# Kernel tuning notes

Hardware: AMD Instinct MI355X
Metric: run time of the kernel (lower is better)

The kernel has to match this reference:

```python
import jax, jax.numpy as jnp
import numpy as np

BOOST_STRENGTH = 1.0  # from init kwargs, already >= 0


def setup_inputs() -> dict:
    key = jax.random.key(0)
    k1, k2 = jax.random.split(key)
    B, C, H, W = 64, 128, 56, 56
    x = jax.random.normal(k1, (B, C, H, W), dtype=jnp.float32)
    # duty cycles are running activation frequencies in [0, 1]
    duty_cycles = jax.random.uniform(k2, (1, C, 1, 1), dtype=jnp.float32)
    k = 40141  # round(0.1 * C*H*W)
    return {"x": x, "duty_cycles": duty_cycles, "k": k}


def reference(x, duty_cycles, k):
    B = x.shape[0]
    n = x.shape[1] * x.shape[2] * x.shape[3]
    target_density = jnp.float32(k / n)
    # boosting only selects winners; original (unboosted) values are kept
    boost_factors = jnp.exp((target_density - duty_cycles) * BOOST_STRENGTH)
    boosted = (x * boost_factors).reshape(B, -1)   # [B, n]
    flat_x = x.reshape(B, -1)                      # [B, n]
    _, idx = jax.lax.top_k(boosted, k)             # [B, k]
    winners = jnp.take_along_axis(flat_x, idx, axis=1)  # original values at winning units
    res = jnp.zeros_like(flat_x).at[jnp.arange(B)[:, None], idx].set(winners)
    return res.reshape(x.shape)
```

## Files before the change

kernel.cpp:

```cpp
#include <hip/hip_runtime.h>
#include <stdint.h>

#define BB 64
#define CC 128
#define HW 3136
#define NPR (CC * HW)
#define NBINS 8192
#define BIN_SHIFT 19
#define KEY_LOW 0x7FFFFu

typedef float vf4 __attribute__((ext_vector_type(4)));

#define ROWMETA_OFF 512
#define COUNTER_OFF 2048
#define HIST_OFF 4096
#define CAND_OFF (HIST_OFF + (size_t)BB * NBINS * 4)

__device__ __forceinline__ uint32_t tokey(float b) {
    uint32_t u = __float_as_uint(b);
    return u ^ (uint32_t)(((int32_t)u >> 31) | 0x80000000);
}

__device__ __forceinline__ float boostf(const float* dc, int c, int K) {
    float td = (float)((double)K / (double)NPR);
    float d = td - dc[c];
    return (float)exp((double)d);
}

__global__ __launch_bounds__(256) void k_hist(const float* __restrict__ x,
                                              const float* __restrict__ dc,
                                              const int* __restrict__ kptr,
                                              uint32_t* __restrict__ hist) {
    __shared__ uint32_t lh[NBINS];
    __shared__ float sbf[8];
    for (int i = threadIdx.x; i < NBINS; i += 256) lh[i] = 0;
    if (threadIdx.x < 8) {
        int c0 = (blockIdx.x & 15) * 8;
        sbf[threadIdx.x] = boostf(dc, c0 + threadIdx.x, *kptr);
    }
    __syncthreads();

    int row = blockIdx.x >> 4;
    int c0 = (blockIdx.x & 15) * 8;
    const float4* xp = (const float4*)(x + (size_t)row * NPR + (size_t)c0 * HW);
    const int nf4 = 8 * HW / 4;

    int t = threadIdx.x;
    for (; t + 256 < nf4; t += 512) {
        float4 a = xp[t];
        float4 b = xp[t + 256];
        float fa = sbf[t / 784];
        float fb = sbf[(t + 256) / 784];
        atomicAdd(&lh[tokey(a.x * fa) >> BIN_SHIFT], 1u);
        atomicAdd(&lh[tokey(a.y * fa) >> BIN_SHIFT], 1u);
        atomicAdd(&lh[tokey(a.z * fa) >> BIN_SHIFT], 1u);
        atomicAdd(&lh[tokey(a.w * fa) >> BIN_SHIFT], 1u);
        atomicAdd(&lh[tokey(b.x * fb) >> BIN_SHIFT], 1u);
        atomicAdd(&lh[tokey(b.y * fb) >> BIN_SHIFT], 1u);
        atomicAdd(&lh[tokey(b.z * fb) >> BIN_SHIFT], 1u);
        atomicAdd(&lh[tokey(b.w * fb) >> BIN_SHIFT], 1u);
    }
    if (t < nf4) {
        float4 a = xp[t];
        float fa = sbf[t / 784];
        atomicAdd(&lh[tokey(a.x * fa) >> BIN_SHIFT], 1u);
        atomicAdd(&lh[tokey(a.y * fa) >> BIN_SHIFT], 1u);
        atomicAdd(&lh[tokey(a.z * fa) >> BIN_SHIFT], 1u);
        atomicAdd(&lh[tokey(a.w * fa) >> BIN_SHIFT], 1u);
    }
    __syncthreads();
    uint32_t* gh = hist + (size_t)row * NBINS;
    for (int i = threadIdx.x; i < NBINS; i += 256) {
        uint32_t v = lh[i];
        if (v) atomicAdd(&gh[i], v);
    }
}

__global__ __launch_bounds__(256) void k_scan(const uint32_t* __restrict__ hist,
                                              const int* __restrict__ kptr,
                                              int2* __restrict__ rowmeta) {
    int row = blockIdx.x;
    const uint32_t* gh = hist + (size_t)row * NBINS;
    uint32_t K = (uint32_t)(*kptr);
    __shared__ uint32_t csum[256];
    int t = threadIdx.x;
    int hi = NBINS - 1 - 32 * t;
    uint32_t s = 0;
    for (int j = 0; j < 32; j++) s += gh[hi - j];
    csum[t] = s;
    __syncthreads();
    for (int off = 1; off < 256; off <<= 1) {
        uint32_t v = (t >= off) ? csum[t - off] : 0u;
        __syncthreads();
        csum[t] += v;
        __syncthreads();
    }
    uint32_t incl = csum[t];
    uint32_t excl = incl - s;
    if (excl < K && incl >= K) {
        uint32_t cum = excl;
        for (int j = 0; j < 32; j++) {
            int b = hi - j;
            uint32_t h = gh[b];
            if (cum + h >= K) { rowmeta[row] = make_int2(b, (int)(K - cum)); break; }
            cum += h;
        }
    }
}

__global__ __launch_bounds__(256) void k_write(const float* __restrict__ x,
                                               const float* __restrict__ dc,
                                               const int* __restrict__ kptr,
                                               const int2* __restrict__ rowmeta,
                                               float* __restrict__ out,
                                               unsigned long long* __restrict__ cand,
                                               uint32_t* __restrict__ counters,
                                               int cap) {
    int row = blockIdx.x >> 4;
    int c0 = (blockIdx.x & 15) * 8;
    int bstar = rowmeta[row].x;

    __shared__ float sbf[8];
    __shared__ uint32_t lcnt;
    __shared__ uint32_t gbase;
    __shared__ unsigned long long lbuf[2048];
    if (threadIdx.x == 0) lcnt = 0;
    if (threadIdx.x < 8) sbf[threadIdx.x] = boostf(dc, c0 + threadIdx.x, *kptr);
    __syncthreads();

    size_t base = (size_t)row * NPR + (size_t)c0 * HW;
    const float4* xp = (const float4*)(x + base);
    vf4* op = (vf4*)(out + base);
    int jbase = c0 * HW;
    const int nf4 = 8 * HW / 4;

    int t = threadIdx.x;
    for (; t + 256 < nf4; t += 512) {
        float4 a = xp[t];
        float4 b = xp[t + 256];
        float fa = sbf[t / 784];
        float fb = sbf[(t + 256) / 784];
        vf4 oa, ob;
        float* ai = (float*)&a;
        float* bi = (float*)&b;
        #pragma unroll
        for (int q = 0; q < 4; q++) {
            float xv = ai[q];
            uint32_t key = tokey(xv * fa);
            int bin = (int)(key >> BIN_SHIFT);
            oa[q] = (bin > bstar) ? xv : 0.0f;
            if (bin == bstar) {
                uint32_t j = (uint32_t)(jbase + 4 * t + q);
                unsigned long long packed =
                    ((unsigned long long)(key & KEY_LOW) << 32) | (uint32_t)(~j);
                uint32_t pos = atomicAdd(&lcnt, 1u);
                if (pos < 2048u) lbuf[pos] = packed;
                else {
                    uint32_t gp = atomicAdd(&counters[row], 1u);
                    if ((int)gp < cap) cand[(size_t)row * cap + gp] = packed;
                }
            }
        }
        #pragma unroll
        for (int q = 0; q < 4; q++) {
            float xv = bi[q];
            uint32_t key = tokey(xv * fb);
            int bin = (int)(key >> BIN_SHIFT);
            ob[q] = (bin > bstar) ? xv : 0.0f;
            if (bin == bstar) {
                uint32_t j = (uint32_t)(jbase + 4 * (t + 256) + q);
                unsigned long long packed =
                    ((unsigned long long)(key & KEY_LOW) << 32) | (uint32_t)(~j);
                uint32_t pos = atomicAdd(&lcnt, 1u);
                if (pos < 2048u) lbuf[pos] = packed;
                else {
                    uint32_t gp = atomicAdd(&counters[row], 1u);
                    if ((int)gp < cap) cand[(size_t)row * cap + gp] = packed;
                }
            }
        }
        __builtin_nontemporal_store(oa, &op[t]);
        __builtin_nontemporal_store(ob, &op[t + 256]);
    }
    if (t < nf4) {
        float4 a = xp[t];
        float fa = sbf[t / 784];
        vf4 oa;
        float* ai = (float*)&a;
        #pragma unroll
        for (int q = 0; q < 4; q++) {
            float xv = ai[q];
            uint32_t key = tokey(xv * fa);
            int bin = (int)(key >> BIN_SHIFT);
            oa[q] = (bin > bstar) ? xv : 0.0f;
            if (bin == bstar) {
                uint32_t j = (uint32_t)(jbase + 4 * t + q);
                unsigned long long packed =
                    ((unsigned long long)(key & KEY_LOW) << 32) | (uint32_t)(~j);
                uint32_t pos = atomicAdd(&lcnt, 1u);
                if (pos < 2048u) lbuf[pos] = packed;
                else {
                    uint32_t gp = atomicAdd(&counters[row], 1u);
                    if ((int)gp < cap) cand[(size_t)row * cap + gp] = packed;
                }
            }
        }
        __builtin_nontemporal_store(oa, &op[t]);
    }
    __syncthreads();
    uint32_t m = lcnt < 2048u ? lcnt : 2048u;
    if (threadIdx.x == 0) gbase = atomicAdd(&counters[row], m);
    __syncthreads();
    for (uint32_t i = threadIdx.x; i < m; i += 256) {
        uint32_t pos = gbase + i;
        if ((int)pos < cap) cand[(size_t)row * cap + pos] = lbuf[i];
    }
}

__global__ __launch_bounds__(1024) void k_select(const float* __restrict__ x,
                                                 float* __restrict__ out,
                                                 const unsigned long long* __restrict__ cand,
                                                 const uint32_t* __restrict__ counters,
                                                 const int2* __restrict__ rowmeta,
                                                 int cap) {
    int row = blockIdx.x;
    uint32_t cnt = counters[row];
    if ((int)cnt > cap) cnt = (uint32_t)cap;
    int E = rowmeta[row].y;
    const unsigned long long* cp = cand + (size_t)row * cap;
    int tid = threadIdx.x;

    __shared__ uint32_t hist[256];
    __shared__ uint32_t sufs[256];
    __shared__ unsigned long long buf[6144];
    __shared__ uint32_t scnt;
    __shared__ int sh_d, sh_done;

    unsigned long long prefix = 0ull, mask = 0ull, thr = 0ull;
    uint32_t remaining = (uint32_t)E;
    bool compacted = false;
    uint32_t csize = cnt;
    if (tid == 0) sh_done = 0;

    for (int shift = 48; shift >= 0; shift -= 8) {
        if (tid < 256) hist[tid] = 0;
        __syncthreads();
        if (!compacted) {
            for (uint32_t s = tid; s < cnt; s += 1024) {
                unsigned long long v = cp[s];
                if ((v & mask) == prefix)
                    atomicAdd(&hist[(uint32_t)(v >> shift) & 255u], 1u);
            }
        } else {
            for (uint32_t s = tid; s < csize; s += 1024)
                atomicAdd(&hist[(uint32_t)(buf[s] >> shift) & 255u], 1u);
        }
        __syncthreads();
        if (tid < 256) sufs[tid] = hist[tid];
        __syncthreads();
        for (int off = 1; off < 256; off <<= 1) {
            uint32_t add = 0;
            if (tid < 256 && tid + off < 256) add = sufs[tid + off];
            __syncthreads();
            if (tid < 256) sufs[tid] += add;
            __syncthreads();
        }
        if (tid < 256) {
            uint32_t sd = sufs[tid];
            uint32_t sn = (tid < 255) ? sufs[tid + 1] : 0u;
            if (sd >= remaining && sn < remaining) sh_d = tid;
        }
        __syncthreads();
        int d = sh_d;
        uint32_t cumG = (d < 255) ? sufs[d + 1] : 0u;
        uint32_t binC = sufs[d] - cumG;
        unsigned long long npref = prefix | ((unsigned long long)(uint32_t)d << shift);
        bool done = (sufs[d] == remaining);
        if (done) {
            thr = npref;
            if (tid == 0) sh_done = 1;
        }
        remaining -= cumG;
        __syncthreads();
        if (!sh_done && binC <= 6144u && shift > 0) {
            if (tid == 0) scnt = 0;
            unsigned long long keep[6]; int nk = 0;
            if (compacted) {
                for (uint32_t s = tid; s < csize; s += 1024) {
                    unsigned long long v = buf[s];
                    if (((uint32_t)(v >> shift) & 255u) == (uint32_t)d) {
                        if (nk < 6) keep[nk++] = v;
                    }
                }
            }
            __syncthreads();
            if (!compacted) {
                for (uint32_t s = tid; s < cnt; s += 1024) {
                    unsigned long long v = cp[s];
                    if ((v & mask) == prefix &&
                        ((uint32_t)(v >> shift) & 255u) == (uint32_t)d) {
                        uint32_t p = atomicAdd(&scnt, 1u);
                        buf[p] = v;
                    }
                }
            } else if (nk > 0) {
                uint32_t p = atomicAdd(&scnt, (uint32_t)nk);
                for (int i = 0; i < nk; i++) buf[p + i] = keep[i];
            }
            __syncthreads();
            csize = binC;
            compacted = true;
        }
        prefix = npref;
        mask |= (0xFFull << shift);
        if (sh_done) break;
    }
    if (!sh_done) thr = prefix;

    const float* xr = x + (size_t)row * NPR;
    float* orow = out + (size_t)row * NPR;
    for (uint32_t s = tid; s < cnt; s += 1024) {
        unsigned long long v = cp[s];
        if (v >= thr) {
            uint32_t j = ~(uint32_t)v;
            orow[j] = xr[j];
        }
    }
}

extern "C" void kernel_launch(void* const* d_in, const int* in_sizes, int n_in,
                              void* d_out, int out_size, void* d_ws, size_t ws_size,
                              hipStream_t stream) {
    const float* x  = (const float*)d_in[0];
    const float* dc = (const float*)d_in[1];
    const int* kptr = (const int*)d_in[2];
    float* out = (float*)d_out;

    char* ws = (char*)d_ws;
    int2* rowmeta       = (int2*)(ws + ROWMETA_OFF);
    uint32_t* counters  = (uint32_t*)(ws + COUNTER_OFF);
    uint32_t* hist      = (uint32_t*)(ws + HIST_OFF);
    unsigned long long* cand = (unsigned long long*)(ws + CAND_OFF);

    size_t cap_sz = (ws_size > CAND_OFF) ? (ws_size - CAND_OFF) / ((size_t)BB * 8) : 0;
    if (cap_sz > 65536) cap_sz = 65536;
    int cap = (int)cap_sz;

    (void)hipMemsetAsync(ws, 0, CAND_OFF, stream);
    k_hist<<<BB * 16, 256, 0, stream>>>(x, dc, kptr, hist);
    k_scan<<<BB, 256, 0, stream>>>(hist, kptr, rowmeta);
    k_write<<<BB * 16, 256, 0, stream>>>(x, dc, kptr, rowmeta, out, cand, counters, cap);
    k_select<<<BB, 1024, 0, stream>>>(x, out, cand, counters, rowmeta, cap);
}
```

Baseline: 243.2 us.

## Fuse histogram, scan, write and select into one cooperative kernel

Replaces the memset plus four separate kernel launches with a single cooperative kernel that uses grid-wide syncs between phases: zeroing, histogram, per-row threshold scan, masked write, and radix select. It removes the launch gaps and the separate memset, and reuses one shared-memory union across phases. The select phase now runs with 256 threads and a smaller compaction buffer instead of 1024 threads, and grid.sync costs plus an occupancy limit of 1024 co-resident blocks are added. If the cooperative launch fails, the code falls back to the old path.

Result: slower. 611.2 us (+151.3%).

```diff
diff --git a/kernel.cpp b/kernel.cpp
--- a/kernel.cpp
+++ b/kernel.cpp
@@ -1,5 +1,8 @@
 #include <hip/hip_runtime.h>
+#include <hip/hip_cooperative_groups.h>
 #include <stdint.h>
+
+namespace cg = cooperative_groups;
 
 #define BB 64
 #define CC 128
@@ -8,6 +11,8 @@
 #define NBINS 8192
 #define BIN_SHIFT 19
 #define KEY_LOW 0x7FFFFu
+#define GRID (BB * 16)
+#define SELCAP 4096
 
 typedef float vf4 __attribute__((ext_vector_type(4)));
 
@@ -25,6 +30,285 @@
     float td = (float)((double)K / (double)NPR);
     float d = td - dc[c];
     return (float)exp((double)d);
+}
+
+union SMem {
+    struct { uint32_t lh[NBINS]; float sbf[8]; } h;
+    struct { uint32_t csum[256]; } sc;
+    struct { float sbf[8]; uint32_t lcnt, gbase;
+             unsigned long long lbuf[2048]; } w;
+    struct { uint32_t hist[256]; uint32_t sufs[256];
+             unsigned long long buf[SELCAP];
+             uint32_t scnt; int sh_d, sh_done; } s;
+};
+
+__global__ __launch_bounds__(256, 4) void k_fused(const float* __restrict__ x,
+                                                  const float* __restrict__ dc,
+                                                  const int* __restrict__ kptr,
+                                                  float* __restrict__ out,
+                                                  unsigned long long* __restrict__ cand,
+                                                  uint32_t* __restrict__ counters,
+                                                  uint32_t* __restrict__ hist,
+                                                  int2* __restrict__ rowmeta,
+                                                  int cap) {
+    cg::grid_group grid = cg::this_grid();
+    __shared__ SMem sm;
+    const int tid = threadIdx.x;
+    const int blk = blockIdx.x;
+    const int row = blk >> 4;
+    const int c0 = (blk & 15) * 8;
+    const int K = *kptr;
+    const int nf4 = 8 * HW / 4;
+
+    {
+        const int total = BB * NBINS;
+        for (int i = blk * 256 + tid; i < total; i += GRID * 256) hist[i] = 0;
+        if (blk == 0 && tid < BB) { counters[tid] = 0u; rowmeta[tid] = make_int2(0, 0); }
+    }
+    grid.sync();
+
+    {
+        for (int i = tid; i < NBINS; i += 256) sm.h.lh[i] = 0;
+        if (tid < 8) sm.h.sbf[tid] = boostf(dc, c0 + tid, K);
+        __syncthreads();
+        const float4* xp = (const float4*)(x + (size_t)row * NPR + (size_t)c0 * HW);
+        int t = tid;
+        for (; t + 256 < nf4; t += 512) {
+            float4 a = xp[t];
+            float4 b = xp[t + 256];
+            float fa = sm.h.sbf[t / 784];
+            float fb = sm.h.sbf[(t + 256) / 784];
+            atomicAdd(&sm.h.lh[tokey(a.x * fa) >> BIN_SHIFT], 1u);
+            atomicAdd(&sm.h.lh[tokey(a.y * fa) >> BIN_SHIFT], 1u);
+            atomicAdd(&sm.h.lh[tokey(a.z * fa) >> BIN_SHIFT], 1u);
+            atomicAdd(&sm.h.lh[tokey(a.w * fa) >> BIN_SHIFT], 1u);
+            atomicAdd(&sm.h.lh[tokey(b.x * fb) >> BIN_SHIFT], 1u);
+            atomicAdd(&sm.h.lh[tokey(b.y * fb) >> BIN_SHIFT], 1u);
+            atomicAdd(&sm.h.lh[tokey(b.z * fb) >> BIN_SHIFT], 1u);
+            atomicAdd(&sm.h.lh[tokey(b.w * fb) >> BIN_SHIFT], 1u);
+        }
+        if (t < nf4) {
+            float4 a = xp[t];
+            float fa = sm.h.sbf[t / 784];
+            atomicAdd(&sm.h.lh[tokey(a.x * fa) >> BIN_SHIFT], 1u);
+            atomicAdd(&sm.h.lh[tokey(a.y * fa) >> BIN_SHIFT], 1u);
+            atomicAdd(&sm.h.lh[tokey(a.z * fa) >> BIN_SHIFT], 1u);
+            atomicAdd(&sm.h.lh[tokey(a.w * fa) >> BIN_SHIFT], 1u);
+        }
+        __syncthreads();
+        uint32_t* gh = hist + (size_t)row * NBINS;
+        for (int i = tid; i < NBINS; i += 256) {
+            uint32_t v = sm.h.lh[i];
+            if (v) atomicAdd(&gh[i], v);
+        }
+    }
+    grid.sync();
+
+    if (blk < BB) {
+        const uint32_t* gh = hist + (size_t)blk * NBINS;
+        uint32_t Ku = (uint32_t)K;
+        int hi = NBINS - 1 - 32 * tid;
+        uint32_t ssum = 0;
+        for (int j = 0; j < 32; j++) ssum += gh[hi - j];
+        sm.sc.csum[tid] = ssum;
+        __syncthreads();
+        for (int off = 1; off < 256; off <<= 1) {
+            uint32_t v = (tid >= off) ? sm.sc.csum[tid - off] : 0u;
+            __syncthreads();
+            sm.sc.csum[tid] += v;
+            __syncthreads();
+        }
+        uint32_t incl = sm.sc.csum[tid];
+        uint32_t excl = incl - ssum;
+        if (excl < Ku && incl >= Ku) {
+            uint32_t cum = excl;
+            for (int j = 0; j < 32; j++) {
+                int b = hi - j;
+                uint32_t h = gh[b];
+                if (cum + h >= Ku) { rowmeta[blk] = make_int2(b, (int)(Ku - cum)); break; }
+                cum += h;
+            }
+        }
+    }
+    grid.sync();
+
+    {
+        int bstar = rowmeta[row].x;
+        if (tid == 0) sm.w.lcnt = 0;
+        if (tid < 8) sm.w.sbf[tid] = boostf(dc, c0 + tid, K);
+        __syncthreads();
+
+        size_t base = (size_t)row * NPR + (size_t)c0 * HW;
+        const float4* xp = (const float4*)(x + base);
+        vf4* op = (vf4*)(out + base);
+        int jbase = c0 * HW;
+
+        int t = tid;
+        for (; t + 256 < nf4; t += 512) {
+            float4 a = xp[t];
+            float4 b = xp[t + 256];
+            float fa = sm.w.sbf[t / 784];
+            float fb = sm.w.sbf[(t + 256) / 784];
+            vf4 oa, ob;
+            float* ai = (float*)&a;
+            float* bi = (float*)&b;
+            #pragma unroll
+            for (int q = 0; q < 4; q++) {
+                float xv = ai[q];
+                uint32_t key = tokey(xv * fa);
+                int bin = (int)(key >> BIN_SHIFT);
+                oa[q] = (bin > bstar) ? xv : 0.0f;
+                if (bin == bstar) {
+                    uint32_t j = (uint32_t)(jbase + 4 * t + q);
+                    unsigned long long packed =
+                        ((unsigned long long)(key & KEY_LOW) << 32) | (uint32_t)(~j);
+                    uint32_t pos = atomicAdd(&sm.w.lcnt, 1u);
+                    if (pos < 2048u) sm.w.lbuf[pos] = packed;
+                    else {
+                        uint32_t gp = atomicAdd(&counters[row], 1u);
+                        if ((int)gp < cap) cand[(size_t)row * cap + gp] = packed;
+                    }
+                }
+            }
+            #pragma unroll
+            for (int q = 0; q < 4; q++) {
+                float xv = bi[q];
+                uint32_t key = tokey(xv * fb);
+                int bin = (int)(key >> BIN_SHIFT);
+                ob[q] = (bin > bstar) ? xv : 0.0f;
+                if (bin == bstar) {
+                    uint32_t j = (uint32_t)(jbase + 4 * (t + 256) + q);
+                    unsigned long long packed =
+                        ((unsigned long long)(key & KEY_LOW) << 32) | (uint32_t)(~j);
+                    uint32_t pos = atomicAdd(&sm.w.lcnt, 1u);
+                    if (pos < 2048u) sm.w.lbuf[pos] = packed;
+                    else {
+                        uint32_t gp = atomicAdd(&counters[row], 1u);
+                        if ((int)gp < cap) cand[(size_t)row * cap + gp] = packed;
+                    }
+                }
+            }
+            __builtin_nontemporal_store(oa, &op[t]);
+            __builtin_nontemporal_store(ob, &op[t + 256]);
+        }
+        if (t < nf4) {
+            float4 a = xp[t];
+            float fa = sm.w.sbf[t / 784];
+            vf4 oa;
+            float* ai = (float*)&a;
+            #pragma unroll
+            for (int q = 0; q < 4; q++) {
+                float xv = ai[q];
+                uint32_t key = tokey(xv * fa);
+                int bin = (int)(key >> BIN_SHIFT);
+                oa[q] = (bin > bstar) ? xv : 0.0f;
+                if (bin == bstar) {
+                    uint32_t j = (uint32_t)(jbase + 4 * t + q);
+                    unsigned long long packed =
+                        ((unsigned long long)(key & KEY_LOW) << 32) | (uint32_t)(~j);
+                    uint32_t pos = atomicAdd(&sm.w.lcnt, 1u);
+                    if (pos < 2048u) sm.w.lbuf[pos] = packed;
+                    else {
+                        uint32_t gp = atomicAdd(&counters[row], 1u);
+                        if ((int)gp < cap) cand[(size_t)row * cap + gp] = packed;
+                    }
+                }
+            }
+            __builtin_nontemporal_store(oa, &op[t]);
+        }
+        __syncthreads();
+        uint32_t m = sm.w.lcnt < 2048u ? sm.w.lcnt : 2048u;
+        if (tid == 0) sm.w.gbase = atomicAdd(&counters[row], m);
+        __syncthreads();
+        for (uint32_t i = tid; i < m; i += 256) {
+            uint32_t pos = sm.w.gbase + i;
+            if ((int)pos < cap) cand[(size_t)row * cap + pos] = sm.w.lbuf[i];
+        }
+    }
+    grid.sync();
+
+    if (blk < BB) {
+        uint32_t cnt = counters[blk];
+        if ((int)cnt > cap) cnt = (uint32_t)cap;
+        int E = rowmeta[blk].y;
+        const unsigned long long* cp = cand + (size_t)blk * cap;
+
+        unsigned long long prefix = 0ull, mask = 0ull, thr = 0ull;
+        uint32_t remaining = (uint32_t)E;
+        bool compacted = false;
+        uint32_t csize = cnt;
+        if (tid == 0) sm.s.sh_done = 0;
+
+        for (int shift = 48; shift >= 0; shift -= 8) {
+            sm.s.hist[tid] = 0;
+            __syncthreads();
+            if (!compacted) {
+                for (uint32_t s = tid; s < cnt; s += 256) {
+                    unsigned long long v = cp[s];
+                    if ((v & mask) == prefix)
+                        atomicAdd(&sm.s.hist[(uint32_t)(v >> shift) & 255u], 1u);
+                }
+            } else {
+                for (uint32_t s = tid; s < csize; s += 256)
+                    atomicAdd(&sm.s.hist[(uint32_t)(sm.s.buf[s] >> shift) & 255u], 1u);
+            }
+            __syncthreads();
+            sm.s.sufs[tid] = sm.s.hist[tid];
+            __syncthreads();
+            for (int off = 1; off < 256; off <<= 1) {
+                uint32_t add = (tid + off < 256) ? sm.s.sufs[tid + off] : 0u;
+                __syncthreads();
+                sm.s.sufs[tid] += add;
+                __syncthreads();
+            }
+            {
+                uint32_t sd = sm.s.sufs[tid];
+                uint32_t sn = (tid < 255) ? sm.s.sufs[tid + 1] : 0u;
+                if (sd >= remaining && sn < remaining) sm.s.sh_d = tid;
+            }
+            __syncthreads();
+            int d = sm.s.sh_d;
+            uint32_t cumG = (d < 255) ? sm.s.sufs[d + 1] : 0u;
+            uint32_t binC = sm.s.sufs[d] - cumG;
+            unsigned long long npref = prefix | ((unsigned long long)(uint32_t)d << shift);
+            unsigned long long nmask = mask | (0xFFull << shift);
+            bool done = (sm.s.sufs[d] == remaining);
+            if (done) {
+                thr = npref;
+                if (tid == 0) sm.s.sh_done = 1;
+            }
+            remaining -= cumG;
+            __syncthreads();
+            if (!sm.s.sh_done && binC <= (uint32_t)SELCAP && shift > 0) {
+                if (tid == 0) sm.s.scnt = 0;
+                __syncthreads();
+                for (uint32_t s = tid; s < cnt; s += 256) {
+                    unsigned long long v = cp[s];
+                    if ((v & nmask) == npref) {
+                        uint32_t p = atomicAdd(&sm.s.scnt, 1u);
+                        sm.s.buf[p] = v;
+                    }
+                }
+                __syncthreads();
+                csize = binC;
+                compacted = true;
+            }
+            prefix = npref;
+            mask = nmask;
+            if (sm.s.sh_done) break;
+        }
+        if (!sm.s.sh_done) thr = prefix;
+
+        const float* xr = x + (size_t)blk * NPR;
+        float* orow = out + (size_t)blk * NPR;
+        for (uint32_t s = tid; s < cnt; s += 256) {
+            unsigned long long v = cp[s];
+            if (v >= thr) {
+                uint32_t j = ~(uint32_t)v;
+                orow[j] = xr[j];
+            }
+        }
+    }
 }
 
 __global__ __launch_bounds__(256) void k_hist(const float* __restrict__ x,
@@ -39,12 +323,10 @@
         sbf[threadIdx.x] = boostf(dc, c0 + threadIdx.x, *kptr);
     }
     __syncthreads();
-
     int row = blockIdx.x >> 4;
     int c0 = (blockIdx.x & 15) * 8;
     const float4* xp = (const float4*)(x + (size_t)row * NPR + (size_t)c0 * HW);
     const int nf4 = 8 * HW / 4;
-
     int t = threadIdx.x;
     for (; t + 256 < nf4; t += 512) {
         float4 a = xp[t];
@@ -119,7 +401,6 @@
     int row = blockIdx.x >> 4;
     int c0 = (blockIdx.x & 15) * 8;
     int bstar = rowmeta[row].x;
-
     __shared__ float sbf[8];
     __shared__ uint32_t lcnt;
     __shared__ uint32_t gbase;
@@ -127,13 +408,11 @@
     if (threadIdx.x == 0) lcnt = 0;
     if (threadIdx.x < 8) sbf[threadIdx.x] = boostf(dc, c0 + threadIdx.x, *kptr);
     __syncthreads();
-
     size_t base = (size_t)row * NPR + (size_t)c0 * HW;
     const float4* xp = (const float4*)(x + base);
     vf4* op = (vf4*)(out + base);
     int jbase = c0 * HW;
     const int nf4 = 8 * HW / 4;
-
     int t = threadIdx.x;
     for (; t + 256 < nf4; t += 512) {
         float4 a = xp[t];
@@ -229,19 +508,16 @@
     int E = rowmeta[row].y;
     const unsigned long long* cp = cand + (size_t)row * cap;
     int tid = threadIdx.x;
-
     __shared__ uint32_t hist[256];
     __shared__ uint32_t sufs[256];
     __shared__ unsigned long long buf[6144];
     __shared__ uint32_t scnt;
     __shared__ int sh_d, sh_done;
-
     unsigned long long prefix = 0ull, mask = 0ull, thr = 0ull;
     uint32_t remaining = (uint32_t)E;
     bool compacted = false;
     uint32_t csize = cnt;
     if (tid == 0) sh_done = 0;
-
     for (int shift = 48; shift >= 0; shift -= 8) {
         if (tid < 256) hist[tid] = 0;
         __syncthreads();
@@ -316,7 +592,6 @@
         if (sh_done) break;
     }
     if (!sh_done) thr = prefix;
-
     const float* xr = x + (size_t)row * NPR;
     float* orow = out + (size_t)row * NPR;
     for (uint32_t s = tid; s < cnt; s += 1024) {
@@ -346,9 +621,15 @@
     if (cap_sz > 65536) cap_sz = 65536;
     int cap = (int)cap_sz;
 
-    (void)hipMemsetAsync(ws, 0, CAND_OFF, stream);
-    k_hist<<<BB * 16, 256, 0, stream>>>(x, dc, kptr, hist);
-    k_scan<<<BB, 256, 0, stream>>>(hist, kptr, rowmeta);
-    k_write<<<BB * 16, 256, 0, stream>>>(x, dc, kptr, rowmeta, out, cand, counters, cap);
-    k_select<<<BB, 1024, 0, stream>>>(x, out, cand, counters, rowmeta, cap);
-}
+    void* args[] = {(void*)&x, (void*)&dc, (void*)&kptr, (void*)&out, (void*)&cand,
+                    (void*)&counters, (void*)&hist, (void*)&rowmeta, (void*)&cap};
+    hipError_t err = hipLaunchCooperativeKernel((void*)k_fused, dim3(GRID), dim3(256),
+                                                args, 0, stream);
+    if (err != hipSuccess) {
+        (void)hipMemsetAsync(ws, 0, CAND_OFF, stream);
+        k_hist<<<BB * 16, 256, 0, stream>>>(x, dc, kptr, hist);
+        k_scan<<<BB, 256, 0, stream>>>(hist, kptr, rowmeta);
+        k_write<<<BB * 16, 256, 0, stream>>>(x, dc, kptr, rowmeta, out, cand, counters, cap);
+        k_select<<<BB, 1024, 0, stream>>>(x, out, cand, counters, rowmeta, cap);
+    }
+}
```

## Fuse scan into histogram and selection into write via last-block completion counters

Applied to the files above, without the earlier changes.

Merges the per-row scan into the histogram kernel and the candidate radix-select into the write kernel. Per-row arrival counters with threadfence let the last of each row's 16 blocks do the follow-up step, cutting the launch count from four to two. The local histogram also packs two 16-bit bins per 32-bit word, halving shared memory, and the select stage now runs in 256 threads with a smaller 2048-entry compaction buffer. The trade-off is that the tail work for a row runs in one 256-thread block instead of a 1024-thread block, and more often has to re-read candidates from global memory.

New measurement: 391.7 us. 61.0% more time.

```diff
diff --git a/kernel.cpp b/kernel.cpp
--- a/kernel.cpp
+++ b/kernel.cpp
@@ -8,11 +8,14 @@
 #define NBINS 8192
 #define BIN_SHIFT 19
 #define KEY_LOW 0x7FFFFu
+#define SELCAP 2048
 
 typedef float vf4 __attribute__((ext_vector_type(4)));
 
 #define ROWMETA_OFF 512
+#define HARR_OFF 1536
 #define COUNTER_OFF 2048
+#define WARR_OFF 2560
 #define HIST_OFF 4096
 #define CAND_OFF (HIST_OFF + (size_t)BB * NBINS * 4)
 
@@ -27,105 +30,121 @@
     return (float)exp((double)d);
 }
 
-__global__ __launch_bounds__(256) void k_hist(const float* __restrict__ x,
-                                              const float* __restrict__ dc,
-                                              const int* __restrict__ kptr,
-                                              uint32_t* __restrict__ hist) {
-    __shared__ uint32_t lh[NBINS];
+__device__ __forceinline__ uint32_t aload32(const uint32_t* p) {
+    return __hip_atomic_load(p, __ATOMIC_RELAXED, __HIP_MEMORY_SCOPE_AGENT);
+}
+__device__ __forceinline__ unsigned long long aload64(const unsigned long long* p) {
+    return __hip_atomic_load(p, __ATOMIC_RELAXED, __HIP_MEMORY_SCOPE_AGENT);
+}
+__device__ __forceinline__ void astore64(unsigned long long* p, unsigned long long v) {
+    __hip_atomic_store(p, v, __ATOMIC_RELAXED, __HIP_MEMORY_SCOPE_AGENT);
+}
+
+__global__ __launch_bounds__(256) void k_hist_scan(const float* __restrict__ x,
+                                                   const float* __restrict__ dc,
+                                                   const int* __restrict__ kptr,
+                                                   uint32_t* __restrict__ hist,
+                                                   uint32_t* __restrict__ harr,
+                                                   int2* __restrict__ rowmeta) {
+    __shared__ uint32_t lh32[NBINS / 2];
     __shared__ float sbf[8];
-    for (int i = threadIdx.x; i < NBINS; i += 256) lh[i] = 0;
-    if (threadIdx.x < 8) {
-        int c0 = (blockIdx.x & 15) * 8;
-        sbf[threadIdx.x] = boostf(dc, c0 + threadIdx.x, *kptr);
-    }
-    __syncthreads();
-
-    int row = blockIdx.x >> 4;
-    int c0 = (blockIdx.x & 15) * 8;
+    __shared__ int lastflag;
+    const int tid = threadIdx.x;
+    const int row = blockIdx.x >> 4;
+    const int c0 = (blockIdx.x & 15) * 8;
+    const int K = *kptr;
+
+    for (int i = tid; i < NBINS / 2; i += 256) lh32[i] = 0;
+    if (tid < 8) sbf[tid] = boostf(dc, c0 + tid, K);
+    __syncthreads();
+
     const float4* xp = (const float4*)(x + (size_t)row * NPR + (size_t)c0 * HW);
     const int nf4 = 8 * HW / 4;
-
-    int t = threadIdx.x;
+    int t = tid;
     for (; t + 256 < nf4; t += 512) {
         float4 a = xp[t];
         float4 b = xp[t + 256];
         float fa = sbf[t / 784];
         float fb = sbf[(t + 256) / 784];
-        atomicAdd(&lh[tokey(a.x * fa) >> BIN_SHIFT], 1u);
-        atomicAdd(&lh[tokey(a.y * fa) >> BIN_SHIFT], 1u);
-        atomicAdd(&lh[tokey(a.z * fa) >> BIN_SHIFT], 1u);
-        atomicAdd(&lh[tokey(a.w * fa) >> BIN_SHIFT], 1u);
-        atomicAdd(&lh[tokey(b.x * fb) >> BIN_SHIFT], 1u);
-        atomicAdd(&lh[tokey(b.y * fb) >> BIN_SHIFT], 1u);
-        atomicAdd(&lh[tokey(b.z * fb) >> BIN_SHIFT], 1u);
-        atomicAdd(&lh[tokey(b.w * fb) >> BIN_SHIFT], 1u);
+        uint32_t bx;
+        bx = tokey(a.x * fa) >> BIN_SHIFT; atomicAdd(&lh32[bx >> 1], 1u << ((bx & 1) << 4));
+        bx = tokey(a.y * fa) >> BIN_SHIFT; atomicAdd(&lh32[bx >> 1], 1u << ((bx & 1) << 4));
+        bx = tokey(a.z * fa) >> BIN_SHIFT; atomicAdd(&lh32[bx >> 1], 1u << ((bx & 1) << 4));
+        bx = tokey(a.w * fa) >> BIN_SHIFT; atomicAdd(&lh32[bx >> 1], 1u << ((bx & 1) << 4));
+        bx = tokey(b.x * fb) >> BIN_SHIFT; atomicAdd(&lh32[bx >> 1], 1u << ((bx & 1) << 4));
+        bx = tokey(b.y * fb) >> BIN_SHIFT; atomicAdd(&lh32[bx >> 1], 1u << ((bx & 1) << 4));
+        bx = tokey(b.z * fb) >> BIN_SHIFT; atomicAdd(&lh32[bx >> 1], 1u << ((bx & 1) << 4));
+        bx = tokey(b.w * fb) >> BIN_SHIFT; atomicAdd(&lh32[bx >> 1], 1u << ((bx & 1) << 4));
     }
     if (t < nf4) {
         float4 a = xp[t];
         float fa = sbf[t / 784];
-        atomicAdd(&lh[tokey(a.x * fa) >> BIN_SHIFT], 1u);
-        atomicAdd(&lh[tokey(a.y * fa) >> BIN_SHIFT], 1u);
-        atomicAdd(&lh[tokey(a.z * fa) >> BIN_SHIFT], 1u);
-        atomicAdd(&lh[tokey(a.w * fa) >> BIN_SHIFT], 1u);
+        uint32_t bx;
+        bx = tokey(a.x * fa) >> BIN_SHIFT; atomicAdd(&lh32[bx >> 1], 1u << ((bx & 1) << 4));
+        bx = tokey(a.y * fa) >> BIN_SHIFT; atomicAdd(&lh32[bx >> 1], 1u << ((bx & 1) << 4));
+        bx = tokey(a.z * fa) >> BIN_SHIFT; atomicAdd(&lh32[bx >> 1], 1u << ((bx & 1) << 4));
+        bx = tokey(a.w * fa) >> BIN_SHIFT; atomicAdd(&lh32[bx >> 1], 1u << ((bx & 1) << 4));
     }
     __syncthreads();
     uint32_t* gh = hist + (size_t)row * NBINS;
-    for (int i = threadIdx.x; i < NBINS; i += 256) {
-        uint32_t v = lh[i];
-        if (v) atomicAdd(&gh[i], v);
-    }
-}
-
-__global__ __launch_bounds__(256) void k_scan(const uint32_t* __restrict__ hist,
-                                              const int* __restrict__ kptr,
-                                              int2* __restrict__ rowmeta) {
-    int row = blockIdx.x;
-    const uint32_t* gh = hist + (size_t)row * NBINS;
-    uint32_t K = (uint32_t)(*kptr);
-    __shared__ uint32_t csum[256];
-    int t = threadIdx.x;
-    int hi = NBINS - 1 - 32 * t;
-    uint32_t s = 0;
-    for (int j = 0; j < 32; j++) s += gh[hi - j];
-    csum[t] = s;
+    for (int i = tid; i < NBINS / 2; i += 256) {
+        uint32_t w = lh32[i];
+        if (w & 0xFFFFu) atomicAdd(&gh[2 * i], w & 0xFFFFu);
+        if (w >> 16)     atomicAdd(&gh[2 * i + 1], w >> 16);
+    }
+    __threadfence();
+    if (tid == 0) lastflag = (atomicAdd(&harr[row], 1u) == 15u);
+    __syncthreads();
+    if (!lastflag) return;
+
+    uint32_t* csum = lh32;
+    uint32_t Ku = (uint32_t)K;
+    int hi = NBINS - 1 - 32 * tid;
+    uint32_t ssum = 0;
+    for (int j = 0; j < 32; j++) ssum += aload32(&gh[hi - j]);
+    csum[tid] = ssum;
     __syncthreads();
     for (int off = 1; off < 256; off <<= 1) {
-        uint32_t v = (t >= off) ? csum[t - off] : 0u;
-        __syncthreads();
-        csum[t] += v;
-        __syncthreads();
-    }
-    uint32_t incl = csum[t];
-    uint32_t excl = incl - s;
-    if (excl < K && incl >= K) {
+        uint32_t v = (tid >= off) ? csum[tid - off] : 0u;
+        __syncthreads();
+        csum[tid] += v;
+        __syncthreads();
+    }
+    uint32_t incl = csum[tid];
+    uint32_t excl = incl - ssum;
+    if (excl < Ku && incl >= Ku) {
         uint32_t cum = excl;
         for (int j = 0; j < 32; j++) {
             int b = hi - j;
-            uint32_t h = gh[b];
-            if (cum + h >= K) { rowmeta[row] = make_int2(b, (int)(K - cum)); break; }
+            uint32_t h = aload32(&gh[b]);
+            if (cum + h >= Ku) { rowmeta[row] = make_int2(b, (int)(Ku - cum)); break; }
             cum += h;
         }
     }
 }
 
-__global__ __launch_bounds__(256) void k_write(const float* __restrict__ x,
-                                               const float* __restrict__ dc,
-                                               const int* __restrict__ kptr,
-                                               const int2* __restrict__ rowmeta,
-                                               float* __restrict__ out,
-                                               unsigned long long* __restrict__ cand,
-                                               uint32_t* __restrict__ counters,
-                                               int cap) {
-    int row = blockIdx.x >> 4;
-    int c0 = (blockIdx.x & 15) * 8;
-    int bstar = rowmeta[row].x;
+__global__ __launch_bounds__(256) void k_write_sel(const float* __restrict__ x,
+                                                   const float* __restrict__ dc,
+                                                   const int* __restrict__ kptr,
+                                                   const int2* __restrict__ rowmeta,
+                                                   float* __restrict__ out,
+                                                   unsigned long long* __restrict__ cand,
+                                                   uint32_t* __restrict__ counters,
+                                                   uint32_t* __restrict__ warr,
+                                                   int cap) {
+    const int tid = threadIdx.x;
+    const int row = blockIdx.x >> 4;
+    const int c0 = (blockIdx.x & 15) * 8;
+    const int bstar = rowmeta[row].x;
 
     __shared__ float sbf[8];
-    __shared__ uint32_t lcnt;
-    __shared__ uint32_t gbase;
-    __shared__ unsigned long long lbuf[2048];
-    if (threadIdx.x == 0) lcnt = 0;
-    if (threadIdx.x < 8) sbf[threadIdx.x] = boostf(dc, c0 + threadIdx.x, *kptr);
+    __shared__ uint32_t lcnt, gbase;
+    __shared__ unsigned long long lbuf[SELCAP];
+    __shared__ uint32_t shist[256], ssufs[256];
+    __shared__ uint32_t scnt;
+    __shared__ int sh_d, sh_done, lastflag;
+    if (tid == 0) lcnt = 0;
+    if (tid < 8) sbf[tid] = boostf(dc, c0 + tid, *kptr);
     __syncthreads();
 
     size_t base = (size_t)row * NPR + (size_t)c0 * HW;
@@ -134,7 +153,7 @@
     int jbase = c0 * HW;
     const int nf4 = 8 * HW / 4;
 
-    int t = threadIdx.x;
+    int t = tid;
     for (; t + 256 < nf4; t += 512) {
         float4 a = xp[t];
         float4 b = xp[t + 256];
@@ -154,10 +173,10 @@
                 unsigned long long packed =
                     ((unsigned long long)(key & KEY_LOW) << 32) | (uint32_t)(~j);
                 uint32_t pos = atomicAdd(&lcnt, 1u);
-                if (pos < 2048u) lbuf[pos] = packed;
+                if (pos < (uint32_t)SELCAP) lbuf[pos] = packed;
                 else {
                     uint32_t gp = atomicAdd(&counters[row], 1u);
-                    if ((int)gp < cap) cand[(size_t)row * cap + gp] = packed;
+                    if ((int)gp < cap) astore64(&cand[(size_t)row * cap + gp], packed);
                 }
             }
         }
@@ -172,10 +191,10 @@
                 unsigned long long packed =
                     ((unsigned long long)(key & KEY_LOW) << 32) | (uint32_t)(~j);
                 uint32_t pos = atomicAdd(&lcnt, 1u);
-                if (pos < 2048u) lbuf[pos] = packed;
+                if (pos < (uint32_t)SELCAP) lbuf[pos] = packed;
                 else {
                     uint32_t gp = atomicAdd(&counters[row], 1u);
-                    if ((int)gp < cap) cand[(size_t)row * cap + gp] = packed;
+                    if ((int)gp < cap) astore64(&cand[(size_t)row * cap + gp], packed);
                 }
             }
         }
@@ -198,43 +217,32 @@
                 unsigned long long packed =
                     ((unsigned long long)(key & KEY_LOW) << 32) | (uint32_t)(~j);
                 uint32_t pos = atomicAdd(&lcnt, 1u);
-                if (pos < 2048u) lbuf[pos] = packed;
+                if (pos < (uint32_t)SELCAP) lbuf[pos] = packed;
                 else {
                     uint32_t gp = atomicAdd(&counters[row], 1u);
-                    if ((int)gp < cap) cand[(size_t)row * cap + gp] = packed;
+                    if ((int)gp < cap) astore64(&cand[(size_t)row * cap + gp], packed);
                 }
             }
         }
         __builtin_nontemporal_store(oa, &op[t]);
     }
     __syncthreads();
-    uint32_t m = lcnt < 2048u ? lcnt : 2048u;
-    if (threadIdx.x == 0) gbase = atomicAdd(&counters[row], m);
-    __syncthreads();
-    for (uint32_t i = threadIdx.x; i < m; i += 256) {
+    uint32_t m = lcnt < (uint32_t)SELCAP ? lcnt : (uint32_t)SELCAP;
+    if (tid == 0) gbase = atomicAdd(&counters[row], m);
+    __syncthreads();
+    for (uint32_t i = tid; i < m; i += 256) {
         uint32_t pos = gbase + i;
-        if ((int)pos < cap) cand[(size_t)row * cap + pos] = lbuf[i];
-    }
-}
-
-__global__ __launch_bounds__(1024) void k_select(const float* __restrict__ x,
-                                                 float* __restrict__ out,
-                                                 const unsigned long long* __restrict__ cand,
-                                                 const uint32_t* __restrict__ counters,
-                                                 const int2* __restrict__ rowmeta,
-                                                 int cap) {
-    int row = blockIdx.x;
-    uint32_t cnt = counters[row];
+        if ((int)pos < cap) astore64(&cand[(size_t)row * cap + pos], lbuf[i]);
+    }
+    __threadfence();
+    if (tid == 0) lastflag = (atomicAdd(&warr[row], 1u) == 15u);
+    __syncthreads();
+    if (!lastflag) return;
+
+    uint32_t cnt = aload32(&counters[row]);
     if ((int)cnt > cap) cnt = (uint32_t)cap;
     int E = rowmeta[row].y;
     const unsigned long long* cp = cand + (size_t)row * cap;
-    int tid = threadIdx.x;
-
-    __shared__ uint32_t hist[256];
-    __shared__ uint32_t sufs[256];
-    __shared__ unsigned long long buf[6144];
-    __shared__ uint32_t scnt;
-    __shared__ int sh_d, sh_done;
 
     unsigned long long prefix = 0ull, mask = 0ull, thr = 0ull;
     uint32_t remaining = (uint32_t)E;
@@ -243,84 +251,69 @@
     if (tid == 0) sh_done = 0;
 
     for (int shift = 48; shift >= 0; shift -= 8) {
-        if (tid < 256) hist[tid] = 0;
+        shist[tid] = 0;
         __syncthreads();
         if (!compacted) {
-            for (uint32_t s = tid; s < cnt; s += 1024) {
-                unsigned long long v = cp[s];
+            for (uint32_t s = tid; s < cnt; s += 256) {
+                unsigned long long v = aload64(&cp[s]);
                 if ((v & mask) == prefix)
-                    atomicAdd(&hist[(uint32_t)(v >> shift) & 255u], 1u);
+                    atomicAdd(&shist[(uint32_t)(v >> shift) & 255u], 1u);
             }
         } else {
-            for (uint32_t s = tid; s < csize; s += 1024)
-                atomicAdd(&hist[(uint32_t)(buf[s] >> shift) & 255u], 1u);
-        }
-        __syncthreads();
-        if (tid < 256) sufs[tid] = hist[tid];
+            for (uint32_t s = tid; s < csize; s += 256)
+                atomicAdd(&shist[(uint32_t)(lbuf[s] >> shift) & 255u], 1u);
+        }
+        __syncthreads();
+        ssufs[tid] = shist[tid];
         __syncthreads();
         for (int off = 1; off < 256; off <<= 1) {
-            uint32_t add = 0;
-            if (tid < 256 && tid + off < 256) add = sufs[tid + off];
+            uint32_t add = (tid + off < 256) ? ssufs[tid + off] : 0u;
             __syncthreads();
-            if (tid < 256) sufs[tid] += add;
+            ssufs[tid] += add;
             __syncthreads();
         }
-        if (tid < 256) {
-            uint32_t sd = sufs[tid];
-            uint32_t sn = (tid < 255) ? sufs[tid + 1] : 0u;
+        {
+            uint32_t sd = ssufs[tid];
+            uint32_t sn = (tid < 255) ? ssufs[tid + 1] : 0u;
             if (sd >= remaining && sn < remaining) sh_d = tid;
         }
         __syncthreads();
         int d = sh_d;
-        uint32_t cumG = (d < 255) ? sufs[d + 1] : 0u;
-        uint32_t binC = sufs[d] - cumG;
+        uint32_t cumG = (d < 255) ? ssufs[d + 1] : 0u;
+        uint32_t binC = ssufs[d] - cumG;
         unsigned long long npref = prefix | ((unsigned long long)(uint32_t)d << shift);
-        bool done = (sufs[d] == remaining);
+        unsigned long long nmask = mask | (0xFFull << shift);
+        bool done = (ssufs[d] == remaining);
         if (done) {
             thr = npref;
             if (tid == 0) sh_done = 1;
         }
         remaining -= cumG;
         __syncthreads();
-        if (!sh_done && binC <= 6144u && shift > 0) {
+        if (!sh_done && binC <= (uint32_t)SELCAP && shift > 0) {
             if (tid == 0) scnt = 0;
-            unsigned long long keep[6]; int nk = 0;
-            if (compacted) {
-                for (uint32_t s = tid; s < csize; s += 1024) {
-                    unsigned long long v = buf[s];
-                    if (((uint32_t)(v >> shift) & 255u) == (uint32_t)d) {
-                        if (nk < 6) keep[nk++] = v;
-                    }
+            __syncthreads();
+            for (uint32_t s = tid; s < cnt; s += 256) {
+                unsigned long long v = aload64(&cp[s]);
+                if ((v & nmask) == npref) {
+                    uint32_t p = atomicAdd(&scnt, 1u);
+                    lbuf[p] = v;
                 }
-            }
-            __syncthreads();
-            if (!compacted) {
-                for (uint32_t s = tid; s < cnt; s += 1024) {
-                    unsigned long long v = cp[s];
-                    if ((v & mask) == prefix &&
-                        ((uint32_t)(v >> shift) & 255u) == (uint32_t)d) {
-                        uint32_t p = atomicAdd(&scnt, 1u);
-                        buf[p] = v;
-                    }
-                }
-            } else if (nk > 0) {
-                uint32_t p = atomicAdd(&scnt, (uint32_t)nk);
-                for (int i = 0; i < nk; i++) buf[p + i] = keep[i];
             }
             __syncthreads();
             csize = binC;
             compacted = true;
         }
         prefix = npref;
-        mask |= (0xFFull << shift);
+        mask = nmask;
         if (sh_done) break;
     }
     if (!sh_done) thr = prefix;
 
     const float* xr = x + (size_t)row * NPR;
     float* orow = out + (size_t)row * NPR;
-    for (uint32_t s = tid; s < cnt; s += 1024) {
-        unsigned long long v = cp[s];
+    for (uint32_t s = tid; s < cnt; s += 256) {
+        unsigned long long v = aload64(&cp[s]);
         if (v >= thr) {
             uint32_t j = ~(uint32_t)v;
             orow[j] = xr[j];
@@ -338,7 +331,9 @@
 
     char* ws = (char*)d_ws;
     int2* rowmeta       = (int2*)(ws + ROWMETA_OFF);
+    uint32_t* harr      = (uint32_t*)(ws + HARR_OFF);
     uint32_t* counters  = (uint32_t*)(ws + COUNTER_OFF);
+    uint32_t* warr      = (uint32_t*)(ws + WARR_OFF);
     uint32_t* hist      = (uint32_t*)(ws + HIST_OFF);
     unsigned long long* cand = (unsigned long long*)(ws + CAND_OFF);
 
@@ -347,8 +342,7 @@
     int cap = (int)cap_sz;
 
     (void)hipMemsetAsync(ws, 0, CAND_OFF, stream);
-    k_hist<<<BB * 16, 256, 0, stream>>>(x, dc, kptr, hist);
-    k_scan<<<BB, 256, 0, stream>>>(hist, kptr, rowmeta);
-    k_write<<<BB * 16, 256, 0, stream>>>(x, dc, kptr, rowmeta, out, cand, counters, cap);
-    k_select<<<BB, 1024, 0, stream>>>(x, out, cand, counters, rowmeta, cap);
-}
+    k_hist_scan<<<BB * 16, 256, 0, stream>>>(x, dc, kptr, hist, harr, rowmeta);
+    k_write_sel<<<BB * 16, 256, 0, stream>>>(x, dc, kptr, rowmeta, out, cand,
+                                             counters, warr, cap);
+}
```

## Fuse histogram scan into write kernel and unroll loads by four

Applied to the files above, without the earlier changes.

Removes the separate per-row scan kernel. Each write block now recomputes the row's threshold bin from the global histogram and stores rowmeta only from the first block of each row. The histogram and write loops now issue four float4 loads per iteration instead of two. The select kernel's compaction always refilters from the full candidate list using the extended prefix mask. This saves one launch and a dependency step, but the scan is now repeated 16 times per row and each block holds more registers.

Result: faster. 225.2 us (-7.4%).

```diff
diff --git a/kernel.cpp b/kernel.cpp
--- a/kernel.cpp
+++ b/kernel.cpp
@@ -8,6 +8,8 @@
 #define NBINS 8192
 #define BIN_SHIFT 19
 #define KEY_LOW 0x7FFFFu
+#define NF4 6272
+#define F4CH 784
 
 typedef float vf4 __attribute__((ext_vector_type(4)));
 
@@ -43,30 +45,41 @@
     int row = blockIdx.x >> 4;
     int c0 = (blockIdx.x & 15) * 8;
     const float4* xp = (const float4*)(x + (size_t)row * NPR + (size_t)c0 * HW);
-    const int nf4 = 8 * HW / 4;
 
     int t = threadIdx.x;
-    for (; t + 256 < nf4; t += 512) {
+    for (; t + 768 < NF4; t += 1024) {
+        float4 a0 = xp[t];
+        float4 a1 = xp[t + 256];
+        float4 a2 = xp[t + 512];
+        float4 a3 = xp[t + 768];
+        float f0 = sbf[t / F4CH];
+        float f1 = sbf[(t + 256) / F4CH];
+        float f2 = sbf[(t + 512) / F4CH];
+        float f3 = sbf[(t + 768) / F4CH];
+        atomicAdd(&lh[tokey(a0.x * f0) >> BIN_SHIFT], 1u);
+        atomicAdd(&lh[tokey(a0.y * f0) >> BIN_SHIFT], 1u);
+        atomicAdd(&lh[tokey(a0.z * f0) >> BIN_SHIFT], 1u);
+        atomicAdd(&lh[tokey(a0.w * f0) >> BIN_SHIFT], 1u);
+        atomicAdd(&lh[tokey(a1.x * f1) >> BIN_SHIFT], 1u);
+        atomicAdd(&lh[tokey(a1.y * f1) >> BIN_SHIFT], 1u);
+        atomicAdd(&lh[tokey(a1.z * f1) >> BIN_SHIFT], 1u);
+        atomicAdd(&lh[tokey(a1.w * f1) >> BIN_SHIFT], 1u);
+        atomicAdd(&lh[tokey(a2.x * f2) >> BIN_SHIFT], 1u);
+        atomicAdd(&lh[tokey(a2.y * f2) >> BIN_SHIFT], 1u);
+        atomicAdd(&lh[tokey(a2.z * f2) >> BIN_SHIFT], 1u);
+        atomicAdd(&lh[tokey(a2.w * f2) >> BIN_SHIFT], 1u);
+        atomicAdd(&lh[tokey(a3.x * f3) >> BIN_SHIFT], 1u);
+        atomicAdd(&lh[tokey(a3.y * f3) >> BIN_SHIFT], 1u);
+        atomicAdd(&lh[tokey(a3.z * f3) >> BIN_SHIFT], 1u);
+        atomicAdd(&lh[tokey(a3.w * f3) >> BIN_SHIFT], 1u);
+    }
+    for (; t < NF4; t += 256) {
         float4 a = xp[t];
-        float4 b = xp[t + 256];
-        float fa = sbf[t / 784];
-        float fb = sbf[(t + 256) / 784];
-        atomicAdd(&lh[tokey(a.x * fa) >> BIN_SHIFT], 1u);
-        atomicAdd(&lh[tokey(a.y * fa) >> BIN_SHIFT], 1u);
-        atomicAdd(&lh[tokey(a.z * fa) >> BIN_SHIFT], 1u);
-        atomicAdd(&lh[tokey(a.w * fa) >> BIN_SHIFT], 1u);
-        atomicAdd(&lh[tokey(b.x * fb) >> BIN_SHIFT], 1u);
-        atomicAdd(&lh[tokey(b.y * fb) >> BIN_SHIFT], 1u);
-        atomicAdd(&lh[tokey(b.z * fb) >> BIN_SHIFT], 1u);
-        atomicAdd(&lh[tokey(b.w * fb) >> BIN_SHIFT], 1u);
-    }
-    if (t < nf4) {
-        float4 a = xp[t];
-        float fa = sbf[t / 784];
-        atomicAdd(&lh[tokey(a.x * fa) >> BIN_SHIFT], 1u);
-        atomicAdd(&lh[tokey(a.y * fa) >> BIN_SHIFT], 1u);
-        atomicAdd(&lh[tokey(a.z * fa) >> BIN_SHIFT], 1u);
-        atomicAdd(&lh[tokey(a.w * fa) >> BIN_SHIFT], 1u);
+        float f = sbf[t / F4CH];
+        atomicAdd(&lh[tokey(a.x * f) >> BIN_SHIFT], 1u);
+        atomicAdd(&lh[tokey(a.y * f) >> BIN_SHIFT], 1u);
+        atomicAdd(&lh[tokey(a.z * f) >> BIN_SHIFT], 1u);
+        atomicAdd(&lh[tokey(a.w * f) >> BIN_SHIFT], 1u);
     }
     __syncthreads();
     uint32_t* gh = hist + (size_t)row * NBINS;
@@ -76,142 +89,118 @@
     }
 }
 
-__global__ __launch_bounds__(256) void k_scan(const uint32_t* __restrict__ hist,
-                                              const int* __restrict__ kptr,
-                                              int2* __restrict__ rowmeta) {
-    int row = blockIdx.x;
-    const uint32_t* gh = hist + (size_t)row * NBINS;
-    uint32_t K = (uint32_t)(*kptr);
+__global__ __launch_bounds__(256) void k_write_scan(const float* __restrict__ x,
+                                                    const float* __restrict__ dc,
+                                                    const int* __restrict__ kptr,
+                                                    const uint32_t* __restrict__ hist,
+                                                    int2* __restrict__ rowmeta,
+                                                    float* __restrict__ out,
+                                                    unsigned long long* __restrict__ cand,
+                                                    uint32_t* __restrict__ counters,
+                                                    int cap) {
+    const int tid = threadIdx.x;
+    const int row = blockIdx.x >> 4;
+    const int c0 = (blockIdx.x & 15) * 8;
+    const int K = *kptr;
+
+    __shared__ float sbf[8];
+    __shared__ uint32_t lcnt, gbase;
+    __shared__ unsigned long long lbuf[2048];
     __shared__ uint32_t csum[256];
-    int t = threadIdx.x;
-    int hi = NBINS - 1 - 32 * t;
-    uint32_t s = 0;
-    for (int j = 0; j < 32; j++) s += gh[hi - j];
-    csum[t] = s;
-    __syncthreads();
-    for (int off = 1; off < 256; off <<= 1) {
-        uint32_t v = (t >= off) ? csum[t - off] : 0u;
-        __syncthreads();
-        csum[t] += v;
-        __syncthreads();
-    }
-    uint32_t incl = csum[t];
-    uint32_t excl = incl - s;
-    if (excl < K && incl >= K) {
-        uint32_t cum = excl;
-        for (int j = 0; j < 32; j++) {
-            int b = hi - j;
-            uint32_t h = gh[b];
-            if (cum + h >= K) { rowmeta[row] = make_int2(b, (int)(K - cum)); break; }
-            cum += h;
-        }
-    }
-}
-
-__global__ __launch_bounds__(256) void k_write(const float* __restrict__ x,
-                                               const float* __restrict__ dc,
-                                               const int* __restrict__ kptr,
-                                               const int2* __restrict__ rowmeta,
-                                               float* __restrict__ out,
-                                               unsigned long long* __restrict__ cand,
-                                               uint32_t* __restrict__ counters,
-                                               int cap) {
-    int row = blockIdx.x >> 4;
-    int c0 = (blockIdx.x & 15) * 8;
-    int bstar = rowmeta[row].x;
-
-    __shared__ float sbf[8];
-    __shared__ uint32_t lcnt;
-    __shared__ uint32_t gbase;
-    __shared__ unsigned long long lbuf[2048];
-    if (threadIdx.x == 0) lcnt = 0;
-    if (threadIdx.x < 8) sbf[threadIdx.x] = boostf(dc, c0 + threadIdx.x, *kptr);
-    __syncthreads();
+    __shared__ int2 smeta;
+    if (tid == 0) lcnt = 0;
+    if (tid < 8) sbf[tid] = boostf(dc, c0 + tid, K);
+
+    {
+        const uint32_t* gh = hist + (size_t)row * NBINS;
+        uint32_t Ku = (uint32_t)K;
+        int hi = NBINS - 1 - 32 * tid;
+        uint32_t hv[32];
+        #pragma unroll
+        for (int j = 0; j < 32; j++) hv[j] = gh[hi - j];
+        uint32_t ssum = 0;
+        #pragma unroll
+        for (int j = 0; j < 32; j++) ssum += hv[j];
+        csum[tid] = ssum;
+        __syncthreads();
+        for (int off = 1; off < 256; off <<= 1) {
+            uint32_t v = (tid >= off) ? csum[tid - off] : 0u;
+            __syncthreads();
+            csum[tid] += v;
+            __syncthreads();
+        }
+        uint32_t incl = csum[tid];
+        uint32_t excl = incl - ssum;
+        if (excl < Ku && incl >= Ku) {
+            uint32_t cum = excl;
+            #pragma unroll
+            for (int j = 0; j < 32; j++) {
+                if (cum + hv[j] >= Ku) { smeta = make_int2(hi - j, (int)(Ku - cum)); break; }
+                cum += hv[j];
+            }
+        }
+        __syncthreads();
+    }
+    const int bstar = smeta.x;
+    if (tid == 0 && (blockIdx.x & 15) == 0) rowmeta[row] = smeta;
 
     size_t base = (size_t)row * NPR + (size_t)c0 * HW;
     const float4* xp = (const float4*)(x + base);
     vf4* op = (vf4*)(out + base);
     int jbase = c0 * HW;
-    const int nf4 = 8 * HW / 4;
-
-    int t = threadIdx.x;
-    for (; t + 256 < nf4; t += 512) {
+
+#define PROC4(av, fv, tu)                                                        \
+    do {                                                                         \
+        vf4 oa;                                                                  \
+        float* ai = (float*)&(av);                                               \
+        _Pragma("unroll")                                                        \
+        for (int q = 0; q < 4; q++) {                                            \
+            float xv = ai[q];                                                    \
+            uint32_t key = tokey(xv * (fv));                                     \
+            int bin = (int)(key >> BIN_SHIFT);                                   \
+            oa[q] = (bin > bstar) ? xv : 0.0f;                                   \
+            if (bin == bstar) {                                                  \
+                uint32_t j = (uint32_t)(jbase + 4 * (tu) + q);                   \
+                unsigned long long packed =                                      \
+                    ((unsigned long long)(key & KEY_LOW) << 32) | (uint32_t)(~j);\
+                uint32_t pos = atomicAdd(&lcnt, 1u);                             \
+                if (pos < 2048u) lbuf[pos] = packed;                             \
+                else {                                                           \
+                    uint32_t gp = atomicAdd(&counters[row], 1u);                 \
+                    if ((int)gp < cap) cand[(size_t)row * cap + gp] = packed;    \
+                }                                                                \
+            }                                                                    \
+        }                                                                        \
+        __builtin_nontemporal_store(oa, &op[(tu)]);                              \
+    } while (0)
+
+    int t = tid;
+    for (; t + 768 < NF4; t += 1024) {
+        float4 a0 = xp[t];
+        float4 a1 = xp[t + 256];
+        float4 a2 = xp[t + 512];
+        float4 a3 = xp[t + 768];
+        float f0 = sbf[t / F4CH];
+        float f1 = sbf[(t + 256) / F4CH];
+        float f2 = sbf[(t + 512) / F4CH];
+        float f3 = sbf[(t + 768) / F4CH];
+        PROC4(a0, f0, t);
+        PROC4(a1, f1, t + 256);
+        PROC4(a2, f2, t + 512);
+        PROC4(a3, f3, t + 768);
+    }
+    for (; t < NF4; t += 256) {
         float4 a = xp[t];
-        float4 b = xp[t + 256];
-        float fa = sbf[t / 784];
-        float fb = sbf[(t + 256) / 784];
-        vf4 oa, ob;
-        float* ai = (float*)&a;
-        float* bi = (float*)&b;
-        #pragma unroll
-        for (int q = 0; q < 4; q++) {
-            float xv = ai[q];
-            uint32_t key = tokey(xv * fa);
-            int bin = (int)(key >> BIN_SHIFT);
-            oa[q] = (bin > bstar) ? xv : 0.0f;
-            if (bin == bstar) {
-                uint32_t j = (uint32_t)(jbase + 4 * t + q);
-                unsigned long long packed =
-                    ((unsigned long long)(key & KEY_LOW) << 32) | (uint32_t)(~j);
-                uint32_t pos = atomicAdd(&lcnt, 1u);
-                if (pos < 2048u) lbuf[pos] = packed;
-                else {
-                    uint32_t gp = atomicAdd(&counters[row], 1u);
-                    if ((int)gp < cap) cand[(size_t)row * cap + gp] = packed;
-                }
-            }
-        }
-        #pragma unroll
-        for (int q = 0; q < 4; q++) {
-            float xv = bi[q];
-            uint32_t key = tokey(xv * fb);
-            int bin = (int)(key >> BIN_SHIFT);
-            ob[q] = (bin > bstar) ? xv : 0.0f;
-            if (bin == bstar) {
-                uint32_t j = (uint32_t)(jbase + 4 * (t + 256) + q);
-                unsigned long long packed =
-                    ((unsigned long long)(key & KEY_LOW) << 32) | (uint32_t)(~j);
-                uint32_t pos = atomicAdd(&lcnt, 1u);
-                if (pos < 2048u) lbuf[pos] = packed;
-                else {
-                    uint32_t gp = atomicAdd(&counters[row], 1u);
-                    if ((int)gp < cap) cand[(size_t)row * cap + gp] = packed;
-                }
-            }
-        }
-        __builtin_nontemporal_store(oa, &op[t]);
-        __builtin_nontemporal_store(ob, &op[t + 256]);
-    }
-    if (t < nf4) {
-        float4 a = xp[t];
-        float fa = sbf[t / 784];
-        vf4 oa;
-        float* ai = (float*)&a;
-        #pragma unroll
-        for (int q = 0; q < 4; q++) {
-            float xv = ai[q];
-            uint32_t key = tokey(xv * fa);
-            int bin = (int)(key >> BIN_SHIFT);
-            oa[q] = (bin > bstar) ? xv : 0.0f;
-            if (bin == bstar) {
-                uint32_t j = (uint32_t)(jbase + 4 * t + q);
-                unsigned long long packed =
-                    ((unsigned long long)(key & KEY_LOW) << 32) | (uint32_t)(~j);
-                uint32_t pos = atomicAdd(&lcnt, 1u);
-                if (pos < 2048u) lbuf[pos] = packed;
-                else {
-                    uint32_t gp = atomicAdd(&counters[row], 1u);
-                    if ((int)gp < cap) cand[(size_t)row * cap + gp] = packed;
-                }
-            }
-        }
-        __builtin_nontemporal_store(oa, &op[t]);
-    }
+        float f = sbf[t / F4CH];
+        PROC4(a, f, t);
+    }
+#undef PROC4
+
     __syncthreads();
     uint32_t m = lcnt < 2048u ? lcnt : 2048u;
-    if (threadIdx.x == 0) gbase = atomicAdd(&counters[row], m);
+    if (tid == 0) gbase = atomicAdd(&counters[row], m);
     __syncthreads();
-    for (uint32_t i = threadIdx.x; i < m; i += 256) {
+    for (uint32_t i = tid; i < m; i += 256) {
         uint32_t pos = gbase + i;
         if ((int)pos < cap) cand[(size_t)row * cap + pos] = lbuf[i];
     }
@@ -275,6 +264,7 @@
         uint32_t cumG = (d < 255) ? sufs[d + 1] : 0u;
         uint32_t binC = sufs[d] - cumG;
         unsigned long long npref = prefix | ((unsigned long long)(uint32_t)d << shift);
+        unsigned long long nmask = mask | (0xFFull << shift);
         bool done = (sufs[d] == remaining);
         if (done) {
             thr = npref;
@@ -284,35 +274,20 @@
         __syncthreads();
         if (!sh_done && binC <= 6144u && shift > 0) {
             if (tid == 0) scnt = 0;
-            unsigned long long keep[6]; int nk = 0;
-            if (compacted) {
-                for (uint32_t s = tid; s < csize; s += 1024) {
-                    unsigned long long v = buf[s];
-                    if (((uint32_t)(v >> shift) & 255u) == (uint32_t)d) {
-                        if (nk < 6) keep[nk++] = v;
-                    }
+            __syncthreads();
+            for (uint32_t s = tid; s < cnt; s += 1024) {
+                unsigned long long v = cp[s];
+                if ((v & nmask) == npref) {
+                    uint32_t p = atomicAdd(&scnt, 1u);
+                    buf[p] = v;
                 }
             }
             __syncthreads();
-            if (!compacted) {
-                for (uint32_t s = tid; s < cnt; s += 1024) {
-                    unsigned long long v = cp[s];
-                    if ((v & mask) == prefix &&
-                        ((uint32_t)(v >> shift) & 255u) == (uint32_t)d) {
-                        uint32_t p = atomicAdd(&scnt, 1u);
-                        buf[p] = v;
-                    }
-                }
-            } else if (nk > 0) {
-                uint32_t p = atomicAdd(&scnt, (uint32_t)nk);
-                for (int i = 0; i < nk; i++) buf[p + i] = keep[i];
-            }
-            __syncthreads();
             csize = binC;
             compacted = true;
         }
         prefix = npref;
-        mask |= (0xFFull << shift);
+        mask = nmask;
         if (sh_done) break;
     }
     if (!sh_done) thr = prefix;
@@ -348,7 +323,7 @@
 
     (void)hipMemsetAsync(ws, 0, CAND_OFF, stream);
     k_hist<<<BB * 16, 256, 0, stream>>>(x, dc, kptr, hist);
-    k_scan<<<BB, 256, 0, stream>>>(hist, kptr, rowmeta);
-    k_write<<<BB * 16, 256, 0, stream>>>(x, dc, kptr, rowmeta, out, cand, counters, cap);
+    k_write_scan<<<BB * 16, 256, 0, stream>>>(x, dc, kptr, hist, rowmeta, out,
+                                              cand, counters, cap);
     k_select<<<BB, 1024, 0, stream>>>(x, out, cand, counters, rowmeta, cap);
 }
```
